# Kernel optimization log

Measured on AMD Instinct MI355X. Metric: run time of the kernel, lower is better.

The kernel has to match this reference:

```python
import jax, jax.numpy as jnp
import numpy as np

D = 10000          # hypervector dimensionality (DIMENSIONS in source)
ALPHA = 0.85
MAX_ITER = 100
TOL = 1e-6


def _pagerank(edge_index, num_nodes):
    # sparse column-stochastic adjacency power iteration (faithful to source)
    row, col = edge_index[0], edge_index[1]
    ones = jnp.ones(edge_index.shape[1], dtype=jnp.float32)
    deg = jax.ops.segment_sum(ones, col, num_segments=num_nodes)  # bincount(columns)
    vals = ALPHA / deg[col]                                       # alpha / out-degree per edge
    p = jnp.float32(1.0 / num_nodes)

    def cond(state):
        v, err, i = state
        return jnp.logical_and(i < MAX_ITER, err >= num_nodes * TOL)

    def body(state):
        v, _, i = state
        mv = jax.ops.segment_sum(vals * v[col], row, num_segments=num_nodes)
        v_new = mv + p * (1.0 - ALPHA)
        return (v_new, jnp.abs(v_new - v).sum(), i + 1)

    v0 = jnp.full((num_nodes,), p, dtype=jnp.float32)
    v, _, _ = jax.lax.while_loop(cond, body, (v0, jnp.float32(jnp.inf), jnp.int32(0)))
    return v


def _undirected_unique(edge_index, num_nodes):
    # to_undirected: sort each edge's endpoints then unique columns.
    # jit-safe emulation: sort by scalar key, mask duplicate keys (weight 0).
    ei = jnp.sort(edge_index, axis=0)                 # [2, E], min/max per edge
    keys = ei[0] * num_nodes + ei[1]
    order = jnp.argsort(keys)
    ksort = keys[order]
    first = jnp.concatenate([jnp.ones((1,), bool), ksort[1:] != ksort[:-1]])
    mask = first.astype(jnp.float32)                  # 1.0 for unique edges, 0.0 for dups
    return ei[0][order], ei[1][order], mask


def setup_inputs() -> dict:
    key = jax.random.key(0)
    k1, k2, k3 = jax.random.split(key, 3)
    N, E, C = 2000, 8192, 10
    edge_index = jax.random.randint(k1, (2, E), 0, N, dtype=jnp.int64)
    # torchhd Random embedding: random bipolar {-1, +1} hypervectors
    node_ids_weight = jnp.where(jax.random.uniform(k2, (N, D)) < 0.5, -1.0, 1.0).astype(jnp.float32)
    # source inits classify weight to 0; use small random values so the output is non-degenerate
    classify_weight = jax.random.normal(k3, (C, D), dtype=jnp.float32) * 0.01
    return {"edge_index": edge_index, "node_ids_weight": node_ids_weight,
            "classify_weight": classify_weight, "num_nodes": N}


def reference(edge_index, node_ids_weight, classify_weight, num_nodes):
    pr = _pagerank(edge_index, num_nodes)
    pr_argsort = jnp.argsort(pr)
    # node_id_hvs[pr_argsort] = node_ids.weight[:num_nodes]
    node_id_hvs = jnp.zeros((num_nodes, D), dtype=node_ids_weight.dtype)
    node_id_hvs = node_id_hvs.at[pr_argsort].set(node_ids_weight[:num_nodes])
    row, col, mask = _undirected_unique(edge_index, num_nodes)
    # bind = elementwise multiply (MAP VSA); multiset = sum over (unique) edges
    enc = jnp.einsum('e,ed,ed->d', mask, node_id_hvs[row], node_id_hvs[col])
    return enc @ classify_weight.T   # Linear(D, num_classes, bias=False)
```

## Files before the change

kernel.cpp:

```cpp
#include <hip/hip_runtime.h>
#include <hip/hip_bf16.h>

#define NN 2000
#define NE 8192
#define DIM 10000
#define NCLS 10
#define HASH_SZ 32768
#define WORDS 313
#define ECH 8
#define RBLK 64
#define REGD 12
#define DUMMY 2047

#define WS_K       0
#define WS_ENC     64
#define WS_V       328576
#define WS_RANK    336576
#define WS_PAIRS   344576
#define WS_HASH    377344
#define WS_PACK    508416

#define ZERO_BYTES 40128
#define ZERO_VEC  (ZERO_BYTES / 16)
#define HASH_VEC  (HASH_SZ * 4 / 16)
#define INIT_TOT  (ZERO_VEC + HASH_VEC)
#define FUSE_ITEMS (INIT_TOT + NN * WORDS)
#define FUSE_BLK  ((FUSE_ITEMS + 1023) / 1024)

__device__ __forceinline__ float wave_sum_dpp(float x) {
#define DPPADD(ctrl, rm, bm)                                                     \
  {                                                                              \
    int y_ = __builtin_amdgcn_update_dpp(0, __float_as_int(x), ctrl, rm, bm, false); \
    x = __fadd_rn(x, __int_as_float(y_));                                        \
  }
  DPPADD(0x111, 0xF, 0xF);
  DPPADD(0x112, 0xF, 0xF);
  DPPADD(0x114, 0xF, 0xE);
  DPPADD(0x118, 0xF, 0xC);
  DPPADD(0x142, 0xA, 0xF);
  DPPADD(0x143, 0xC, 0xF);
#undef DPPADD
  return x;
}

__global__ __launch_bounds__(1024) void fused_pre_kernel(const int* __restrict__ eidx,
                                                         const float* __restrict__ W,
                                                         char* __restrict__ ws) {
  if (blockIdx.x != 0) {
    int t = (int)(blockIdx.x - 1) * 1024 + threadIdx.x;
    if (t < ZERO_VEC) {
      reinterpret_cast<uint4*>(ws)[t] = make_uint4(0u, 0u, 0u, 0u);
      return;
    }
    if (t < INIT_TOT) {
      reinterpret_cast<uint4*>(ws + WS_HASH)[t - ZERO_VEC] =
          make_uint4(0xFFFFFFFFu, 0xFFFFFFFFu, 0xFFFFFFFFu, 0xFFFFFFFFu);
      return;
    }
    int j = t - INIT_TOT;
    if (j >= NN * WORDS) return;
    unsigned int* packed = (unsigned int*)(ws + WS_PACK);
    int w = j / NN;
    int node = j - w * NN;
    int d0 = w * 32;
    const float* p = W + (size_t)node * DIM + d0;
    unsigned int m = 0;
    if (d0 + 32 <= DIM) {
#pragma unroll
      for (int q = 0; q < 8; ++q) {
        float4 v4 = *reinterpret_cast<const float4*>(p + q * 4);
        m |= (__float_as_uint(v4.x) >> 31) << (q * 4);
        m |= (__float_as_uint(v4.y) >> 31) << (q * 4 + 1);
        m |= (__float_as_uint(v4.z) >> 31) << (q * 4 + 2);
        m |= (__float_as_uint(v4.w) >> 31) << (q * 4 + 3);
      }
    } else {
      for (int q = 0; q < DIM - d0; ++q) m |= (__float_as_uint(p[q]) >> 31) << q;
    }
    packed[(size_t)w * NN + node] = m;
    return;
  }

  __shared__ unsigned short s_ccol[NE];
  __shared__ unsigned short s_ced[NE];
  __shared__ int s_base[NN + 1];
  __shared__ int s_aux[2048];
  __shared__ int s_w[2048];
  __shared__ float s_wv[2][2048];
  __shared__ float4 s_red4[2][4];
  float* s_redf = (float*)s_red4;
  float* s_val = (float*)s_aux;

  int tid = threadIdx.x;
  int wid = tid >> 6, lane = tid & 63;

  for (int i = tid; i < 2048; i += 1024) { s_w[i] = 0; s_aux[i] = 0; }
  for (int i = NN + tid; i < 2048; i += 1024) { s_wv[0][i] = 0.f; s_wv[1][i] = 0.f; }
  __syncthreads();

  int er[8], ec[8];
#pragma unroll
  for (int k = 0; k < 8; ++k) {
    int e = tid + k * 1024;
    er[k] = eidx[e];
    ec[k] = eidx[NE + e];
    atomicAdd(&s_w[er[k]], 1);
    atomicAdd(&s_aux[ec[k]], 1);
  }
  __syncthreads();

  {
    int n0 = tid, n1 = tid + 1024;
    for (int st = 1; st < 2048; st <<= 1) {
      int v0 = (n0 >= st) ? s_w[n0 - st] : 0;
      int v1 = (n1 >= st) ? s_w[n1 - st] : 0;
      __syncthreads();
      s_w[n0] += v0;
      s_w[n1] += v1;
      __syncthreads();
    }
    if (tid == 0) s_base[0] = 0;
    for (int n = tid; n < NN; n += 1024) s_base[n + 1] = s_w[n];
  }
  __syncthreads();
  for (int i = tid; i < 2048; i += 1024) s_w[i] = 0;
  __syncthreads();

#pragma unroll
  for (int k = 0; k < 8; ++k) {
    int e = tid + k * 1024;
    int r = er[k];
    int slot = s_base[r] + atomicAdd(&s_w[r], 1);
    s_ccol[slot] = (unsigned short)ec[k];
    s_ced[slot] = (unsigned short)e;
  }
  __syncthreads();

  const float p = 0.0005f;
  const float addv = 0.0005f * 0.15f;
  for (int n = tid; n < NN; n += 1024) {
    int s0 = s_base[n], s1 = s_base[n + 1];
    for (int a = s0 + 1; a < s1; ++a) {
      unsigned short ke = s_ced[a], kc = s_ccol[a];
      int b = a - 1;
      while (b >= s0 && s_ced[b] > ke) {
        s_ced[b + 1] = s_ced[b];
        s_ccol[b + 1] = s_ccol[b];
        --b;
      }
      s_ced[b + 1] = ke;
      s_ccol[b + 1] = kc;
    }
    float vv = 0.85f / (float)s_aux[n];
    s_val[n] = vv;
    s_wv[0][n] = __fmul_rn(vv, p);
  }
  __syncthreads();

  int b0s = s_base[tid], b0e = s_base[tid + 1];
  int b1s = 0, b1e = 0;
  bool has1 = (tid + 1024 < NN);
  if (has1) { b1s = s_base[tid + 1024]; b1e = s_base[tid + 1025]; }
  float val0 = s_val[tid];
  float val1 = has1 ? s_val[tid + 1024] : 0.f;
  int c0r[REGD], c1r[REGD];
#pragma unroll
  for (int k = 0; k < REGD; ++k) {
    int i0 = b0s + k;
    c0r[k] = (i0 < b0e) ? (int)s_ccol[min(i0, NE - 1)] : DUMMY;
    int i1 = b1s + k;
    c1r[k] = (has1 && i1 < b1e) ? (int)s_ccol[min(i1, NE - 1)] : DUMMY;
  }
  float vc0 = p, vc1 = p;

  float err = __builtin_inff();
  int it = 0;
  int pb = 0;
  while (it < 100 && err >= 0.002f) {
    const float* wv = s_wv[pb];
    float ep = 0.f;
    float sum = 0.f;
#pragma unroll
    for (int k = 0; k < REGD; ++k) sum = __fadd_rn(sum, wv[c0r[k]]);
    for (int k = b0s + REGD; k < b0e; ++k) sum = __fadd_rn(sum, wv[s_ccol[k]]);
    float vn0 = __fadd_rn(sum, addv);
    ep += fabsf(__fsub_rn(vn0, vc0));
    float vn1 = vc1;
    if (has1) {
      sum = 0.f;
#pragma unroll
      for (int k = 0; k < REGD; ++k) sum = __fadd_rn(sum, wv[c1r[k]]);
      for (int k = b1s + REGD; k < b1e; ++k) sum = __fadd_rn(sum, wv[s_ccol[k]]);
      vn1 = __fadd_rn(sum, addv);
      ep += fabsf(__fsub_rn(vn1, vc1));
    }
    float* wvn = s_wv[pb ^ 1];
    wvn[tid] = __fmul_rn(val0, vn0);
    if (has1) wvn[tid + 1024] = __fmul_rn(val1, vn1);
    vc0 = vn0; vc1 = vn1;
    float wsum = wave_sum_dpp(ep);
    if (lane == 63) s_redf[pb * 16 + wid] = wsum;
    __syncthreads();
    float4 q0 = s_red4[pb][0], q1 = s_red4[pb][1], q2 = s_red4[pb][2], q3 = s_red4[pb][3];
    float t = 0.f;
    t += q0.x; t += q0.y; t += q0.z; t += q0.w;
    t += q1.x; t += q1.y; t += q1.z; t += q1.w;
    t += q2.x; t += q2.y; t += q2.z; t += q2.w;
    t += q3.x; t += q3.y; t += q3.z; t += q3.w;
    err = t;
    pb ^= 1;
    ++it;
  }
  float* vout = (float*)(ws + WS_V);
  vout[tid] = vc0;
  if (has1) vout[tid + 1024] = vc1;
}

__global__ __launch_bounds__(256) void rank_dedup_kernel(const int* __restrict__ eidx,
                                                         char* __restrict__ ws) {
  int tid = threadIdx.x;
  if (blockIdx.x < 32) {
    const float* v = (const float*)(ws + WS_V);
    int* rnk = (int*)(ws + WS_RANK);
    __shared__ float s_v[NN];
    __shared__ int s_part[4][RBLK];
    for (int j = tid; j < NN; j += 256) s_v[j] = v[j];
    __syncthreads();
    int li = tid & (RBLK - 1);
    int seg = tid >> 6;
    int i = blockIdx.x * RBLK + li;
    float vi = (i < NN) ? s_v[i] : 0.f;
    const int jper = NN / 4;
    int j0 = seg * jper, j1 = j0 + jper;
    int r = 0;
    for (int j = j0; j < j1; ++j) {
      float vj = s_v[j];
      r += ((vj < vi) || (vj == vi && j < i)) ? 1 : 0;
    }
    s_part[seg][li] = r;
    __syncthreads();
    if (tid < RBLK) {
      int i2 = blockIdx.x * RBLK + tid;
      if (i2 < NN)
        rnk[i2] = s_part[0][tid] + s_part[1][tid] + s_part[2][tid] + s_part[3][tid];
    }
  } else {
    int* hash = (int*)(ws + WS_HASH);
    unsigned int* pairs = (unsigned int*)(ws + WS_PAIRS);
    int* Kp = (int*)(ws + WS_K);
    int e = (int)(blockIdx.x - 32) * 256 + tid;
    int r = eidx[e], c = eidx[NE + e];
    int a = min(r, c), b = max(r, c);
    int key = a * NN + b;
    unsigned int h = ((unsigned int)key * 2654435761u) >> 17;
    for (;;) {
      h &= (HASH_SZ - 1);
      int old = atomicCAS(&hash[h], -1, key);
      if (old == -1) {
        int idx = atomicAdd(Kp, 1);
        pairs[idx] = ((unsigned int)a << 16) | (unsigned int)b;
        return;
      }
      if (old == key) return;
      ++h;
    }
  }
}

__global__ __launch_bounds__(256) void encpop_kernel(char* __restrict__ ws) {
  const unsigned int* packed = (const unsigned int*)(ws + WS_PACK);
  const unsigned int* pairs = (const unsigned int*)(ws + WS_PAIRS);
  const int* Kp = (const int*)(ws + WS_K);
  const int* rnk_g = (const int*)(ws + WS_RANK);
  int* enc_int = (int*)(ws + WS_ENC);
  __shared__ unsigned short s_rnk[NN];
  __shared__ unsigned int s_col[NN];
  __shared__ int s_part[4][32];
  int w = blockIdx.x;
  int tid = threadIdx.x;
  int wid = tid >> 6, lane = tid & 63;
  for (int i = tid; i < NN; i += 256) s_rnk[i] = (unsigned short)rnk_g[i];
  __syncthreads();
  for (int i = tid; i < NN; i += 256)
    s_col[i] = packed[(size_t)w * NN + s_rnk[i]];
  __syncthreads();
  int K = *Kp;
  const int per = NE / ECH;
  int e0 = blockIdx.y * per;
  int cnt[32];
#pragma unroll
  for (int b = 0; b < 32; ++b) cnt[b] = 0;
  for (int e = e0 + tid; e < e0 + per; e += 256) {
    unsigned int x = 0;
    if (e < K) {
      unsigned int pk = pairs[e];
      x = s_col[pk >> 16] ^ s_col[pk & 0xffffu];
    }
#pragma unroll
    for (int b = 0; b < 32; ++b)
      cnt[b] += (int)__popcll(__ballot(x & (1u << b)));
  }
  if (lane == 0) {
#pragma unroll
    for (int b = 0; b < 32; ++b) s_part[wid][b] = cnt[b];
  }
  __syncthreads();
  if (tid < 32) {
    int tot = s_part[0][tid] + s_part[1][tid] + s_part[2][tid] + s_part[3][tid];
    if (tot) atomicAdd(&enc_int[w * 32 + tid], tot);
  }
}

__global__ __launch_bounds__(256) void out_kernel(const float* __restrict__ Wc,
                                                  char* __restrict__ ws,
                                                  float* __restrict__ out) {
  const int* enc_int = (const int*)(ws + WS_ENC);
  int K = *(const int*)(ws + WS_K);
  __shared__ float red[4];
  int c = blockIdx.x;
  float s = 0.f;
  for (int d = threadIdx.x; d < DIM; d += 256)
    s += (float)(K - 2 * enc_int[d]) * Wc[c * DIM + d];
  for (int o = 32; o > 0; o >>= 1) s += __shfl_down(s, o, 64);
  if ((threadIdx.x & 63) == 0) red[threadIdx.x >> 6] = s;
  __syncthreads();
  if (threadIdx.x == 0) out[c] = red[0] + red[1] + red[2] + red[3];
}

extern "C" void kernel_launch(void* const* d_in, const int* in_sizes, int n_in,
                              void* d_out, int out_size, void* d_ws, size_t ws_size,
                              hipStream_t stream) {
  const int* eidx = (const int*)d_in[0];
  const float* Wn = (const float*)d_in[1];
  const float* Wc = (const float*)d_in[2];
  float* out = (float*)d_out;
  char* ws = (char*)d_ws;

  fused_pre_kernel<<<FUSE_BLK + 1, 1024, 0, stream>>>(eidx, Wn, ws);
  rank_dedup_kernel<<<64, 256, 0, stream>>>(eidx, ws);
  encpop_kernel<<<dim3(WORDS, ECH), 256, 0, stream>>>(ws);
  out_kernel<<<NCLS, 256, 0, stream>>>(Wc, ws, out);
}
```

Measured before the change: 87.01 us.

## Fuse output GEMV into encpop via last-block counter; remap PageRank rows to 512 threads

The separate out_kernel launch is removed. The last encpop block to finish, found through an atomic done-counter, now computes the 10-class dot products, which saves one kernel launch. Separately, the PageRank power iteration now runs on 512 threads owning four rows each instead of 1024 threads owning two rows. This cuts the number of active waves per barrier, but lengthens the serial work per thread and depends on WS_DONE being zeroed by the earlier init.

```diff
diff --git a/kernel.cpp b/kernel.cpp
--- a/kernel.cpp
+++ b/kernel.cpp
@@ -11,8 +11,10 @@
 #define RBLK 64
 #define REGD 12
 #define DUMMY 2047
+#define NTILE (WORDS * ECH)
 
 #define WS_K       0
+#define WS_DONE    8
 #define WS_ENC     64
 #define WS_V       328576
 #define WS_RANK    336576
@@ -157,21 +159,36 @@
   }
   __syncthreads();
 
-  int b0s = s_base[tid], b0e = s_base[tid + 1];
-  int b1s = 0, b1e = 0;
-  bool has1 = (tid + 1024 < NN);
-  if (has1) { b1s = s_base[tid + 1024]; b1e = s_base[tid + 1025]; }
-  float val0 = s_val[tid];
-  float val1 = has1 ? s_val[tid + 1024] : 0.f;
-  int c0r[REGD], c1r[REGD];
+  bool own = (tid < 512);
+  int r0 = tid, r1 = tid + 512, r2 = tid + 1024, r3 = tid + 1536;
+  bool has3 = own && (r3 < NN);
+  int b0s = 0, b0e = 0, b1s = 0, b1e = 0, b2s = 0, b2e = 0, b3s = 0, b3e = 0;
+  float val0 = 0.f, val1 = 0.f, val2 = 0.f, val3 = 0.f;
+  if (own) {
+    b0s = s_base[r0]; b0e = s_base[r0 + 1];
+    b1s = s_base[r1]; b1e = s_base[r1 + 1];
+    b2s = s_base[r2]; b2e = s_base[r2 + 1];
+    val0 = s_val[r0]; val1 = s_val[r1]; val2 = s_val[r2];
+    if (has3) { b3s = s_base[r3]; b3e = s_base[r3 + 1]; val3 = s_val[r3]; }
+  }
+  int c0r[REGD], c1r[REGD], c2r[REGD], c3r[REGD];
 #pragma unroll
   for (int k = 0; k < REGD; ++k) {
-    int i0 = b0s + k;
-    c0r[k] = (i0 < b0e) ? (int)s_ccol[min(i0, NE - 1)] : DUMMY;
-    int i1 = b1s + k;
-    c1r[k] = (has1 && i1 < b1e) ? (int)s_ccol[min(i1, NE - 1)] : DUMMY;
-  }
-  float vc0 = p, vc1 = p;
+    c0r[k] = (own && b0s + k < b0e) ? (int)s_ccol[min(b0s + k, NE - 1)] : DUMMY;
+    c1r[k] = (own && b1s + k < b1e) ? (int)s_ccol[min(b1s + k, NE - 1)] : DUMMY;
+    c2r[k] = (own && b2s + k < b2e) ? (int)s_ccol[min(b2s + k, NE - 1)] : DUMMY;
+    c3r[k] = (has3 && b3s + k < b3e) ? (int)s_ccol[min(b3s + k, NE - 1)] : DUMMY;
+  }
+  float vc0 = p, vc1 = p, vc2 = p, vc3 = p;
+
+#define ROW_SUM(CR, BS, BE, VC, VN)                                            \
+  {                                                                            \
+    float sum = 0.f;                                                           \
+    _Pragma("unroll")                                                          \
+    for (int k = 0; k < REGD; ++k) sum = __fadd_rn(sum, wv[CR[k]]);            \
+    for (int k = (BS) + REGD; k < (BE); ++k) sum = __fadd_rn(sum, wv[s_ccol[k]]); \
+    VN = __fadd_rn(sum, addv);                                                 \
+  }
 
   float err = __builtin_inff();
   int it = 0;
@@ -179,25 +196,19 @@
   while (it < 100 && err >= 0.002f) {
     const float* wv = s_wv[pb];
     float ep = 0.f;
-    float sum = 0.f;
-#pragma unroll
-    for (int k = 0; k < REGD; ++k) sum = __fadd_rn(sum, wv[c0r[k]]);
-    for (int k = b0s + REGD; k < b0e; ++k) sum = __fadd_rn(sum, wv[s_ccol[k]]);
-    float vn0 = __fadd_rn(sum, addv);
-    ep += fabsf(__fsub_rn(vn0, vc0));
-    float vn1 = vc1;
-    if (has1) {
-      sum = 0.f;
-#pragma unroll
-      for (int k = 0; k < REGD; ++k) sum = __fadd_rn(sum, wv[c1r[k]]);
-      for (int k = b1s + REGD; k < b1e; ++k) sum = __fadd_rn(sum, wv[s_ccol[k]]);
-      vn1 = __fadd_rn(sum, addv);
-      ep += fabsf(__fsub_rn(vn1, vc1));
-    }
-    float* wvn = s_wv[pb ^ 1];
-    wvn[tid] = __fmul_rn(val0, vn0);
-    if (has1) wvn[tid + 1024] = __fmul_rn(val1, vn1);
-    vc0 = vn0; vc1 = vn1;
+    float vn0 = vc0, vn1 = vc1, vn2 = vc2, vn3 = vc3;
+    if (own) {
+      ROW_SUM(c0r, b0s, b0e, vc0, vn0); ep += fabsf(__fsub_rn(vn0, vc0));
+      ROW_SUM(c1r, b1s, b1e, vc1, vn1); ep += fabsf(__fsub_rn(vn1, vc1));
+      ROW_SUM(c2r, b2s, b2e, vc2, vn2); ep += fabsf(__fsub_rn(vn2, vc2));
+      if (has3) { ROW_SUM(c3r, b3s, b3e, vc3, vn3); ep += fabsf(__fsub_rn(vn3, vc3)); }
+      float* wvn = s_wv[pb ^ 1];
+      wvn[r0] = __fmul_rn(val0, vn0);
+      wvn[r1] = __fmul_rn(val1, vn1);
+      wvn[r2] = __fmul_rn(val2, vn2);
+      if (has3) wvn[r3] = __fmul_rn(val3, vn3);
+    }
+    vc0 = vn0; vc1 = vn1; vc2 = vn2; vc3 = vn3;
     float wsum = wave_sum_dpp(ep);
     if (lane == 63) s_redf[pb * 16 + wid] = wsum;
     __syncthreads();
@@ -211,9 +222,14 @@
     pb ^= 1;
     ++it;
   }
+#undef ROW_SUM
   float* vout = (float*)(ws + WS_V);
-  vout[tid] = vc0;
-  if (has1) vout[tid + 1024] = vc1;
+  if (own) {
+    vout[r0] = vc0;
+    vout[r1] = vc1;
+    vout[r2] = vc2;
+    if (has3) vout[r3] = vc3;
+  }
 }
 
 __global__ __launch_bounds__(256) void rank_dedup_kernel(const int* __restrict__ eidx,
@@ -267,15 +283,19 @@
   }
 }
 
-__global__ __launch_bounds__(256) void encpop_kernel(char* __restrict__ ws) {
+__global__ __launch_bounds__(256) void encpop_kernel(const float* __restrict__ Wc,
+                                                     char* __restrict__ ws,
+                                                     float* __restrict__ out) {
   const unsigned int* packed = (const unsigned int*)(ws + WS_PACK);
   const unsigned int* pairs = (const unsigned int*)(ws + WS_PAIRS);
   const int* Kp = (const int*)(ws + WS_K);
   const int* rnk_g = (const int*)(ws + WS_RANK);
   int* enc_int = (int*)(ws + WS_ENC);
+  unsigned int* done = (unsigned int*)(ws + WS_DONE);
   __shared__ unsigned short s_rnk[NN];
   __shared__ unsigned int s_col[NN];
   __shared__ int s_part[4][32];
+  __shared__ int s_last;
   int w = blockIdx.x;
   int tid = threadIdx.x;
   int wid = tid >> 6, lane = tid & 63;
@@ -309,22 +329,29 @@
     int tot = s_part[0][tid] + s_part[1][tid] + s_part[2][tid] + s_part[3][tid];
     if (tot) atomicAdd(&enc_int[w * 32 + tid], tot);
   }
-}
-
-__global__ __launch_bounds__(256) void out_kernel(const float* __restrict__ Wc,
-                                                  char* __restrict__ ws,
-                                                  float* __restrict__ out) {
-  const int* enc_int = (const int*)(ws + WS_ENC);
-  int K = *(const int*)(ws + WS_K);
+  __syncthreads();
+  if (tid == 0) {
+    __threadfence();
+    unsigned int prev = __hip_atomic_fetch_add(done, 1u, __ATOMIC_ACQ_REL,
+                                               __HIP_MEMORY_SCOPE_AGENT);
+    s_last = (prev == (unsigned int)(NTILE - 1)) ? 1 : 0;
+  }
+  __syncthreads();
+  if (!s_last) return;
+  __threadfence();
   __shared__ float red[4];
-  int c = blockIdx.x;
-  float s = 0.f;
-  for (int d = threadIdx.x; d < DIM; d += 256)
-    s += (float)(K - 2 * enc_int[d]) * Wc[c * DIM + d];
-  for (int o = 32; o > 0; o >>= 1) s += __shfl_down(s, o, 64);
-  if ((threadIdx.x & 63) == 0) red[threadIdx.x >> 6] = s;
-  __syncthreads();
-  if (threadIdx.x == 0) out[c] = red[0] + red[1] + red[2] + red[3];
+  for (int c = 0; c < NCLS; ++c) {
+    float s = 0.f;
+    for (int d = tid; d < DIM; d += 256) {
+      int cd = __hip_atomic_load(&enc_int[d], __ATOMIC_RELAXED, __HIP_MEMORY_SCOPE_AGENT);
+      s += (float)(K - 2 * cd) * Wc[c * DIM + d];
+    }
+    for (int o = 32; o > 0; o >>= 1) s += __shfl_down(s, o, 64);
+    if ((tid & 63) == 0) red[tid >> 6] = s;
+    __syncthreads();
+    if (tid == 0) out[c] = red[0] + red[1] + red[2] + red[3];
+    __syncthreads();
+  }
 }
 
 extern "C" void kernel_launch(void* const* d_in, const int* in_sizes, int n_in,
@@ -338,6 +365,5 @@
 
   fused_pre_kernel<<<FUSE_BLK + 1, 1024, 0, stream>>>(eidx, Wn, ws);
   rank_dedup_kernel<<<64, 256, 0, stream>>>(eidx, ws);
-  encpop_kernel<<<dim3(WORDS, ECH), 256, 0, stream>>>(ws);
-  out_kernel<<<NCLS, 256, 0, stream>>>(Wc, ws, out);
-}
+  encpop_kernel<<<dim3(WORDS, ECH), 256, 0, stream>>>(Wc, ws, out);
+}
```

New measurement: 248.0 us. +185.0%, slower.
